# Kernel tuning notes

Hardware: AMD Instinct MI355X
Metric: run time of the kernel (lower is better)

## Reference

```python
import jax, jax.numpy as jnp
import numpy as np

B, C, H, W = 64, 256, 64, 64
E = 4                      # num_experts
CELL = 8
OUT = CELL * CELL + 1      # 65
EPS_BN = 1e-5
EPS_LB = 1e-6


def setup_inputs() -> dict:
    key = jax.random.key(0)
    ks = jax.random.split(key, 6)
    x = jax.random.normal(ks[0], (B, C, H, W), dtype=jnp.float32)
    w_experts = jax.random.normal(ks[1], (E, C, OUT), dtype=jnp.float32) * 0.05
    b_experts = jax.random.normal(ks[2], (E, OUT), dtype=jnp.float32) * 0.05
    w_gate = jax.random.normal(ks[3], (C, E), dtype=jnp.float32) * 0.05
    b_gate = jax.random.normal(ks[4], (E,), dtype=jnp.float32) * 0.05
    gamma = jnp.ones((OUT,), dtype=jnp.float32)
    beta = jnp.zeros((OUT,), dtype=jnp.float32)
    return {"x": x, "w_experts": w_experts, "b_experts": b_experts,
            "w_gate": w_gate, "b_gate": b_gate, "gamma": gamma, "beta": beta}


def pixel_shuffle(t, r):
    n, ch, h, w = t.shape
    nc = ch // (r * r)
    t = t.reshape(n, nc, r, r, h, w)
    t = t.transpose(0, 1, 4, 2, 5, 3)
    return t.reshape(n, nc, h * r, w * r)


def reference(x, w_experts, b_experts, w_gate, b_gate, gamma, beta):
    x = jax.nn.relu(x)
    xh = x.transpose(0, 2, 3, 1)                       # [B,H,W,C]

    # gating: global-avg-pool -> linear -> softmax -> hard top-1
    pooled = xh.mean(axis=(1, 2))                      # [B,C]
    gate = jax.nn.softmax(pooled @ w_gate + b_gate, axis=-1)
    idx = jnp.argmax(gate, axis=-1)                    # [B]

    # load-balancing KL(usage || uniform)
    usage = jnp.mean(jax.nn.one_hot(idx, E, dtype=xh.dtype), axis=0) + EPS_LB
    usage = usage / usage.sum()
    lb_loss = jnp.sum(usage * (jnp.log(usage) - jnp.log(jnp.full_like(usage, 1.0 / E))))

    # fused gather->grouped-GEMM (per-sample expert weight selection)
    w_sel = w_experts[idx]                             # [B,C,OUT]
    b_sel = b_experts[idx]                             # [B,OUT]
    y = jnp.einsum('bhwc,bco->bhwo', xh, w_sel) + b_sel[:, None, None, :]
    y = y.transpose(0, 3, 1, 2)                        # [B,OUT,H,W]

    # BatchNorm2d (training mode: batch statistics, biased variance)
    mean = y.mean(axis=(0, 2, 3), keepdims=True)
    var = y.var(axis=(0, 2, 3), keepdims=True)
    logits = (y - mean) / jnp.sqrt(var + EPS_BN)
    logits = logits * gamma[None, :, None, None] + beta[None, :, None, None]

    prob = jax.nn.softmax(logits, axis=1)[:, :-1]      # drop dustbin channel
    prob = pixel_shuffle(prob, CELL)                   # [B,1,H*8,W*8]
    prob = prob[:, 0]                                  # squeeze dim=1
    return logits, prob, lb_loss
```

## Files before the change

kernel.cpp:

```cpp
#include <hip/hip_runtime.h>
#include <stdint.h>
#include <math.h>

#define B_    64
#define C_    256
#define HW_   4096
#define E_    4
#define OUT_  65
#define NPAD_ 80

#define LOGITS_SZ (B_*OUT_*HW_)
#define PROB_SZ   (B_*512*512)

#define POOLED_OFF 0u
#define IDX_OFF    65536u
#define BNSUM_OFF  65792u
#define BNSS_OFF   66112u
#define SCSH_OFF   66432u
#define WT_OFF     67072u
#define YB_OFF     230912u
#define CLEAR_BYTES 66432u

typedef float  f4 __attribute__((ext_vector_type(4)));
typedef short  s8 __attribute__((ext_vector_type(8)));

__device__ __forceinline__ uint32_t f2bf(float f){
  uint32_t u = __float_as_uint(f);
  return (u + 0x7FFFu + ((u >> 16) & 1u)) >> 16;
}
__device__ __forceinline__ uint32_t pk(float lo, float hi){
  return f2bf(lo) | (f2bf(hi) << 16);
}
__device__ __forceinline__ float bf2f(uint32_t u){
  return __uint_as_float((u & 0xFFFFu) << 16);
}

__global__ __launch_bounds__(256) void k_prep(const float* __restrict__ x,
                                              uint16_t* __restrict__ xb,
                                              float* __restrict__ pooled){
  __shared__ float pool_lds[64];
  int bid = blockIdx.x;
  int b = bid >> 7, ct = (bid >> 5) & 3, pt = bid & 31;
  int t = threadIdx.x;
  int cg = t & 7, pgg = t >> 3;
  int c0 = ct*64 + cg*8;
  int p0 = pt*128 + pgg*4;
  if (t < 64) pool_lds[t] = 0.f;
  __syncthreads();

  float v[8][4]; float s[8];
  const float* xp = x + ((size_t)(b*C_ + c0))*HW_ + p0;
#pragma unroll
  for (int r = 0; r < 8; ++r){
    float4 f = *(const float4*)(xp + (size_t)r*HW_);
    v[r][0]=fmaxf(f.x,0.f); v[r][1]=fmaxf(f.y,0.f);
    v[r][2]=fmaxf(f.z,0.f); v[r][3]=fmaxf(f.w,0.f);
    s[r] = v[r][0]+v[r][1]+v[r][2]+v[r][3];
  }
  uint16_t* op = xb + ((size_t)(b*HW_ + p0))*C_ + c0;
#pragma unroll
  for (int p = 0; p < 4; ++p){
    uint4 w;
    w.x = pk(v[0][p], v[1][p]); w.y = pk(v[2][p], v[3][p]);
    w.z = pk(v[4][p], v[5][p]); w.w = pk(v[6][p], v[7][p]);
    *(uint4*)(op + (size_t)p*C_) = w;
  }
#pragma unroll
  for (int r = 0; r < 8; ++r){
    float vv = s[r];
    vv += __shfl_xor(vv, 8);
    vv += __shfl_xor(vv, 16);
    vv += __shfl_xor(vv, 32);
    if ((t & 56) == 0)
      atomicAdd(&pool_lds[cg*8 + r], vv);
  }
  __syncthreads();
  if (t < 64) atomicAdd(pooled + b*C_ + ct*64 + t, pool_lds[t]);
}

__global__ void k_wt(const float* __restrict__ w_experts, uint16_t* __restrict__ Wt){
  int bid = blockIdx.x;
  int e = bid / OUT_, o = bid % OUT_;
  int t = threadIdx.x, c = t*4;
  const float* src = w_experts + (size_t)e*C_*OUT_ + o;
  float a0 = src[(size_t)c*OUT_],     a1 = src[(size_t)(c+1)*OUT_];
  float a2 = src[(size_t)(c+2)*OUT_], a3 = src[(size_t)(c+3)*OUT_];
  uint2 w; w.x = pk(a0,a1); w.y = pk(a2,a3);
  *(uint2*)(Wt + ((size_t)(e*NPAD_ + o))*C_ + c) = w;
}

__global__ void k_gate(const float* __restrict__ pooled_sum,
                       const float* __restrict__ w_gate,
                       const float* __restrict__ b_gate,
                       int* __restrict__ idx_ws, float* __restrict__ out_lb){
  __shared__ float gl[64][4];
  __shared__ int ish[64];
  int t = threadIdx.x;
  int b = t >> 2, e = t & 3;
  float dot = 0.f;
  const float* pr = pooled_sum + b*C_;
  for (int c = 0; c < C_; c += 4){
    float4 p4 = *(const float4*)(pr + c);
    dot += p4.x*w_gate[c*4+e] + p4.y*w_gate[(c+1)*4+e]
         + p4.z*w_gate[(c+2)*4+e] + p4.w*w_gate[(c+3)*4+e];
  }
  gl[b][e] = dot * (1.f/4096.f) + b_gate[e];
  __syncthreads();
  if (t < 64){
    float best = gl[t][0]; int bi = 0;
    for (int ee = 1; ee < 4; ++ee){ float vv = gl[t][ee]; if (vv > best){best = vv; bi = ee;} }
    idx_ws[t] = bi; ish[t] = bi;
  }
  __syncthreads();
  if (t == 0){
    int cnt[4] = {0,0,0,0};
    for (int bb = 0; bb < 64; ++bb) cnt[ish[bb]]++;
    double u[4], S = 0.0;
    for (int ee = 0; ee < 4; ++ee){ u[ee] = cnt[ee]/64.0 + 1e-6; S += u[ee]; }
    double lb = 0.0;
    for (int ee = 0; ee < 4; ++ee){ double uu = u[ee]/S; lb += uu*(log(uu) - log(0.25)); }
    *out_lb = (float)lb;
  }
}

__global__ __launch_bounds__(256) void k_gemm(const uint16_t* __restrict__ xb,
                                              const uint16_t* __restrict__ Wt,
                                              const int* __restrict__ idx_ws,
                                              const float* __restrict__ b_experts,
                                              uint16_t* __restrict__ yb,
                                              float* __restrict__ bnsum,
                                              float* __restrict__ bnss){
  __shared__ float2 bnp[NPAD_*4];
  int bid = blockIdx.x;
  int b = bid >> 4, pt = bid & 15;
  int t = threadIdx.x;
  int w = t >> 6, lane = t & 63;
  int l15 = lane & 15, quad = lane >> 4;
  int e = idx_ws[b];
  int p0 = pt*256 + w*64;
  const uint16_t* ap = xb + ((size_t)(b*HW_ + p0 + l15))*C_ + quad*8;
  const uint16_t* bp = Wt + (size_t)e*NPAD_*C_ + (size_t)l15*C_ + quad*8;

  f4 acc[4][5];
#pragma unroll
  for (int mt=0; mt<4; ++mt)
#pragma unroll
    for (int nt=0; nt<5; ++nt){ f4 z = {0.f,0.f,0.f,0.f}; acc[mt][nt] = z; }

#pragma unroll
  for (int ks = 0; ks < 8; ++ks){
    int ko = ks*32;
    s8 av[4], bv[5];
#pragma unroll
    for (int mt=0; mt<4; ++mt) av[mt] = *(const s8*)(ap + (size_t)mt*16*C_ + ko);
#pragma unroll
    for (int nt=0; nt<5; ++nt) bv[nt] = *(const s8*)(bp + (size_t)nt*16*C_ + ko);
#pragma unroll
    for (int mt=0; mt<4; ++mt)
#pragma unroll
      for (int nt=0; nt<5; ++nt)
        acc[mt][nt] = __builtin_amdgcn_mfma_f32_16x16x32_bf16(av[mt], bv[nt], acc[mt][nt], 0, 0, 0);
  }

#pragma unroll
  for (int nt=0; nt<5; ++nt){
    int o = nt*16 + l15;
    float bias = (o < OUT_) ? b_experts[e*OUT_ + o] : 0.f;
    float s1 = 0.f, s2 = 0.f;
#pragma unroll
    for (int mt=0; mt<4; ++mt){
#pragma unroll
      for (int r=0; r<4; ++r){
        float vv = acc[mt][nt][r] + bias;
        acc[mt][nt][r] = vv;
        s1 += vv; s2 += vv*vv;
      }
      if (o < OUT_){
        size_t base = ((size_t)(b*OUT_ + o))*HW_ + p0 + mt*16 + quad*4;
        uint2 st;
        st.x = pk(acc[mt][nt][0], acc[mt][nt][1]);
        st.y = pk(acc[mt][nt][2], acc[mt][nt][3]);
        *(uint2*)(yb + base) = st;
      }
    }
    s1 += __shfl_xor(s1, 16); s1 += __shfl_xor(s1, 32);
    s2 += __shfl_xor(s2, 16); s2 += __shfl_xor(s2, 32);
    if (quad == 0) bnp[(nt*16 + l15)*4 + w] = make_float2(s1, s2);
  }
  __syncthreads();
  if (t < OUT_){
    float2 a0 = bnp[t*4+0], a1 = bnp[t*4+1], a2 = bnp[t*4+2], a3 = bnp[t*4+3];
    atomicAdd(bnsum + t, a0.x+a1.x+a2.x+a3.x);
    atomicAdd(bnss  + t, a0.y+a1.y+a2.y+a3.y);
  }
}

__global__ void k_stats(const float* __restrict__ bnsum, const float* __restrict__ bnss,
                        const float* __restrict__ gamma, const float* __restrict__ beta,
                        float2* __restrict__ scsh){
  int t = threadIdx.x;
  if (t < OUT_){
    const float invN = 1.f/(float)(B_*HW_);
    float mean = bnsum[t]*invN;
    float var  = bnss[t]*invN - mean*mean;
    float sc   = gamma[t] / sqrtf(var + 1e-5f);
    scsh[t] = make_float2(sc, beta[t] - mean*sc);
  }
}

__global__ __launch_bounds__(256) void k_final(const uint16_t* __restrict__ yb,
                                               const float2* __restrict__ scsh,
                                               float* __restrict__ out_logits,
                                               float* __restrict__ out_prob){
  __shared__ float lt[OUT_*132];
  __shared__ float2 ss[OUT_];
  int bid = blockIdx.x;
  int b = bid >> 5, pt = bid & 31;
  int p0 = pt*128;
  int t = threadIdx.x;
  if (t < OUT_) ss[t] = scsh[t];
  __syncthreads();

  int prr = t & 15, og = t >> 4;
#pragma unroll
  for (int oi = 0; oi < 5; ++oi){
    int o = og + oi*16;
    if (o < OUT_){
      size_t base = ((size_t)(b*OUT_ + o))*HW_ + p0 + prr*8;
      uint4 raw = *(const uint4*)(yb + base);
      float f[8];
      f[0]=bf2f(raw.x); f[1]=bf2f(raw.x>>16);
      f[2]=bf2f(raw.y); f[3]=bf2f(raw.y>>16);
      f[4]=bf2f(raw.z); f[5]=bf2f(raw.z>>16);
      f[6]=bf2f(raw.w); f[7]=bf2f(raw.w>>16);
      float2 sv = ss[o];
#pragma unroll
      for (int k=0;k<8;++k) f[k] = f[k]*sv.x + sv.y;
      float4 w0 = make_float4(f[0],f[1],f[2],f[3]);
      float4 w1 = make_float4(f[4],f[5],f[6],f[7]);
      *(float4*)(out_logits + base)     = w0;
      *(float4*)(out_logits + base + 4) = w1;
      float* lp = lt + o*132 + prr*8;
      *(float4*)(lp)     = w0;
      *(float4*)(lp + 4) = w1;
    }
  }
  __syncthreads();

  if (t < 128){
    float m = -1e30f;
    for (int o = 0; o < OUT_; ++o) m = fmaxf(m, lt[o*132 + t]);
    float ssum = 0.f;
    for (int o = 0; o < OUT_; ++o) ssum += __expf(lt[o*132 + t] - m);
    float inv = 1.f/ssum;
    int P = p0 + t;
    int h = P >> 6, wd = P & 63;
    float* pb = out_prob + ((size_t)b << 18) + (size_t)(h*8)*512 + wd*8;
#pragma unroll
    for (int r1 = 0; r1 < 8; ++r1){
      float4 q0, q1;
      q0.x = __expf(lt[(r1*8+0)*132+t]-m)*inv;
      q0.y = __expf(lt[(r1*8+1)*132+t]-m)*inv;
      q0.z = __expf(lt[(r1*8+2)*132+t]-m)*inv;
      q0.w = __expf(lt[(r1*8+3)*132+t]-m)*inv;
      q1.x = __expf(lt[(r1*8+4)*132+t]-m)*inv;
      q1.y = __expf(lt[(r1*8+5)*132+t]-m)*inv;
      q1.z = __expf(lt[(r1*8+6)*132+t]-m)*inv;
      q1.w = __expf(lt[(r1*8+7)*132+t]-m)*inv;
      *(float4*)(pb + r1*512)     = q0;
      *(float4*)(pb + r1*512 + 4) = q1;
    }
  }
}

extern "C" void kernel_launch(void* const* d_in, const int* in_sizes, int n_in,
                              void* d_out, int out_size, void* d_ws, size_t ws_size,
                              hipStream_t stream){
  const float* x         = (const float*)d_in[0];
  const float* w_experts = (const float*)d_in[1];
  const float* b_experts = (const float*)d_in[2];
  const float* w_gate    = (const float*)d_in[3];
  const float* b_gate    = (const float*)d_in[4];
  const float* gamma     = (const float*)d_in[5];
  const float* beta      = (const float*)d_in[6];

  float* out = (float*)d_out;
  char*  ws  = (char*)d_ws;
  float*     pooled = (float*)(ws + POOLED_OFF);
  int*       idxw   = (int*)(ws + IDX_OFF);
  float*     bnsum  = (float*)(ws + BNSUM_OFF);
  float*     bnss   = (float*)(ws + BNSS_OFF);
  float2*    scsh   = (float2*)(ws + SCSH_OFF);
  uint16_t*  Wt     = (uint16_t*)(ws + WT_OFF);
  uint16_t*  ybm    = (uint16_t*)(ws + YB_OFF);
  uint16_t*  xbm    = (uint16_t*)d_out;

  float* logits = out;
  float* prob   = out + LOGITS_SZ;
  float* lb     = out + LOGITS_SZ + PROB_SZ;

  hipMemsetAsync(ws, 0, CLEAR_BYTES, stream);
  k_prep <<<8192, 256, 0, stream>>>(x, xbm, pooled);
  k_wt   <<<E_*OUT_, 64, 0, stream>>>(w_experts, Wt);
  k_gate <<<1, 256, 0, stream>>>(pooled, w_gate, b_gate, idxw, lb);
  k_gemm <<<1024, 256, 0, stream>>>(xbm, Wt, idxw, b_experts, ybm, bnsum, bnss);
  k_stats<<<1, 128, 0, stream>>>(bnsum, bnss, gamma, beta, scsh);
  k_final<<<2048, 256, 0, stream>>>(ybm, scsh, logits, prob);
}
```

Before: 514.8 us.

## Pre-swizzle GEMM operands into MFMA fragment layout and merge small kernels

Writes the bf16 activations and expert weights in a fragment-major layout, so each wavefront's MFMA operand loads become contiguous 1 KB blocks instead of strided row reads. It also merges the weight-transpose and gating kernels into one launch and folds the BN stats kernel into k_final, removing two launches. The cost is more scattered stores in k_prep and the BN scale/shift being recomputed in every k_final block.

```diff
diff --git a/kernel.cpp b/kernel.cpp
--- a/kernel.cpp
+++ b/kernel.cpp
@@ -16,7 +16,6 @@
 #define IDX_OFF    65536u
 #define BNSUM_OFF  65792u
 #define BNSS_OFF   66112u
-#define SCSH_OFF   66432u
 #define WT_OFF     67072u
 #define YB_OFF     230912u
 #define CLEAR_BYTES 66432u
@@ -34,6 +33,7 @@
 __device__ __forceinline__ float bf2f(uint32_t u){
   return __uint_as_float((u & 0xFFFFu) << 16);
 }
+
 
 __global__ __launch_bounds__(256) void k_prep(const float* __restrict__ x,
                                               uint16_t* __restrict__ xb,
@@ -57,13 +57,17 @@
     v[r][2]=fmaxf(f.z,0.f); v[r][3]=fmaxf(f.w,0.f);
     s[r] = v[r][0]+v[r][1]+v[r][2]+v[r][3];
   }
-  uint16_t* op = xb + ((size_t)(b*HW_ + p0))*C_ + c0;
-#pragma unroll
-  for (int p = 0; p < 4; ++p){
+  int ksg  = ct*2 + (cg >> 2);
+  int quad = cg & 3;
+#pragma unroll
+  for (int pp = 0; pp < 4; ++pp){
+    int p = p0 + pp;
+    uint16_t* dst = xb + ((((size_t)(b*256 + (p>>4))*8 + ksg)*64)
+                          + (size_t)((p&15)*4 + quad))*8;
     uint4 w;
-    w.x = pk(v[0][p], v[1][p]); w.y = pk(v[2][p], v[3][p]);
-    w.z = pk(v[4][p], v[5][p]); w.w = pk(v[6][p], v[7][p]);
-    *(uint4*)(op + (size_t)p*C_) = w;
+    w.x = pk(v[0][pp], v[1][pp]); w.y = pk(v[2][pp], v[3][pp]);
+    w.z = pk(v[4][pp], v[5][pp]); w.w = pk(v[6][pp], v[7][pp]);
+    *(uint4*)dst = w;
   }
 #pragma unroll
   for (int r = 0; r < 8; ++r){
@@ -78,24 +82,39 @@
   if (t < 64) atomicAdd(pooled + b*C_ + ct*64 + t, pool_lds[t]);
 }
 
-__global__ void k_wt(const float* __restrict__ w_experts, uint16_t* __restrict__ Wt){
+__global__ void k_wtgate(const float* __restrict__ w_experts,
+                         const float* __restrict__ w_gate,
+                         const float* __restrict__ b_gate,
+                         const float* __restrict__ pooled_sum,
+                         uint16_t* __restrict__ Wt,
+                         int* __restrict__ idx_ws,
+                         float* __restrict__ out_lb){
   int bid = blockIdx.x;
-  int e = bid / OUT_, o = bid % OUT_;
-  int t = threadIdx.x, c = t*4;
-  const float* src = w_experts + (size_t)e*C_*OUT_ + o;
-  float a0 = src[(size_t)c*OUT_],     a1 = src[(size_t)(c+1)*OUT_];
-  float a2 = src[(size_t)(c+2)*OUT_], a3 = src[(size_t)(c+3)*OUT_];
-  uint2 w; w.x = pk(a0,a1); w.y = pk(a2,a3);
-  *(uint2*)(Wt + ((size_t)(e*NPAD_ + o))*C_ + c) = w;
-}
-
-__global__ void k_gate(const float* __restrict__ pooled_sum,
-                       const float* __restrict__ w_gate,
-                       const float* __restrict__ b_gate,
-                       int* __restrict__ idx_ws, float* __restrict__ out_lb){
+  int t = threadIdx.x;
+  if (bid < 320){
+    if (t >= 32) return;
+    int e = bid / NPAD_, o = bid % NPAD_;
+    int ks = t >> 2, quad = t & 3;
+    int c = t*8;
+    float a[8];
+    if (o < OUT_){
+      const float* src = w_experts + (size_t)e*C_*OUT_ + o;
+#pragma unroll
+      for (int j = 0; j < 8; ++j) a[j] = src[(size_t)(c+j)*OUT_];
+    } else {
+#pragma unroll
+      for (int j = 0; j < 8; ++j) a[j] = 0.f;
+    }
+    uint4 w;
+    w.x = pk(a[0],a[1]); w.y = pk(a[2],a[3]);
+    w.z = pk(a[4],a[5]); w.w = pk(a[6],a[7]);
+    uint16_t* dst = Wt + ((((size_t)(e*5 + (o>>4))*8 + ks)*64)
+                          + (size_t)((o&15)*4 + quad))*8;
+    *(uint4*)dst = w;
+    return;
+  }
   __shared__ float gl[64][4];
   __shared__ int ish[64];
-  int t = threadIdx.x;
   int b = t >> 2, e = t & 3;
   float dot = 0.f;
   const float* pr = pooled_sum + b*C_;
@@ -136,10 +155,11 @@
   int t = threadIdx.x;
   int w = t >> 6, lane = t & 63;
   int l15 = lane & 15, quad = lane >> 4;
+  int lid = l15*4 + quad;
   int e = idx_ws[b];
   int p0 = pt*256 + w*64;
-  const uint16_t* ap = xb + ((size_t)(b*HW_ + p0 + l15))*C_ + quad*8;
-  const uint16_t* bp = Wt + (size_t)e*NPAD_*C_ + (size_t)l15*C_ + quad*8;
+  const uint16_t* ap = xb + ((size_t)(b*256 + pt*16 + w*4))*4096 + (size_t)lid*8;
+  const uint16_t* bp = Wt + (size_t)e*5*4096 + (size_t)lid*8;
 
   f4 acc[4][5];
 #pragma unroll
@@ -149,12 +169,11 @@
 
 #pragma unroll
   for (int ks = 0; ks < 8; ++ks){
-    int ko = ks*32;
     s8 av[4], bv[5];
 #pragma unroll
-    for (int mt=0; mt<4; ++mt) av[mt] = *(const s8*)(ap + (size_t)mt*16*C_ + ko);
-#pragma unroll
-    for (int nt=0; nt<5; ++nt) bv[nt] = *(const s8*)(bp + (size_t)nt*16*C_ + ko);
+    for (int mt=0; mt<4; ++mt) av[mt] = *(const s8*)(ap + (size_t)mt*4096 + ks*512);
+#pragma unroll
+    for (int nt=0; nt<5; ++nt) bv[nt] = *(const s8*)(bp + (size_t)nt*4096 + ks*512);
 #pragma unroll
     for (int mt=0; mt<4; ++mt)
 #pragma unroll
@@ -195,21 +214,11 @@
   }
 }
 
-__global__ void k_stats(const float* __restrict__ bnsum, const float* __restrict__ bnss,
-                        const float* __restrict__ gamma, const float* __restrict__ beta,
-                        float2* __restrict__ scsh){
-  int t = threadIdx.x;
-  if (t < OUT_){
-    const float invN = 1.f/(float)(B_*HW_);
-    float mean = bnsum[t]*invN;
-    float var  = bnss[t]*invN - mean*mean;
-    float sc   = gamma[t] / sqrtf(var + 1e-5f);
-    scsh[t] = make_float2(sc, beta[t] - mean*sc);
-  }
-}
-
 __global__ __launch_bounds__(256) void k_final(const uint16_t* __restrict__ yb,
-                                               const float2* __restrict__ scsh,
+                                               const float* __restrict__ bnsum,
+                                               const float* __restrict__ bnss,
+                                               const float* __restrict__ gamma,
+                                               const float* __restrict__ beta,
                                                float* __restrict__ out_logits,
                                                float* __restrict__ out_prob){
   __shared__ float lt[OUT_*132];
@@ -218,7 +227,13 @@
   int b = bid >> 5, pt = bid & 31;
   int p0 = pt*128;
   int t = threadIdx.x;
-  if (t < OUT_) ss[t] = scsh[t];
+  if (t < OUT_){
+    const float invN = 1.f/(float)(B_*HW_);
+    float mean = bnsum[t]*invN;
+    float var  = bnss[t]*invN - mean*mean;
+    float sc   = gamma[t] / sqrtf(var + 1e-5f);
+    ss[t] = make_float2(sc, beta[t] - mean*sc);
+  }
   __syncthreads();
 
   int prr = t & 15, og = t >> 4;
@@ -290,7 +305,6 @@
   int*       idxw   = (int*)(ws + IDX_OFF);
   float*     bnsum  = (float*)(ws + BNSUM_OFF);
   float*     bnss   = (float*)(ws + BNSS_OFF);
-  float2*    scsh   = (float2*)(ws + SCSH_OFF);
   uint16_t*  Wt     = (uint16_t*)(ws + WT_OFF);
   uint16_t*  ybm    = (uint16_t*)(ws + YB_OFF);
   uint16_t*  xbm    = (uint16_t*)d_out;
@@ -300,10 +314,8 @@
   float* lb     = out + LOGITS_SZ + PROB_SZ;
 
   hipMemsetAsync(ws, 0, CLEAR_BYTES, stream);
-  k_prep <<<8192, 256, 0, stream>>>(x, xbm, pooled);
-  k_wt   <<<E_*OUT_, 64, 0, stream>>>(w_experts, Wt);
-  k_gate <<<1, 256, 0, stream>>>(pooled, w_gate, b_gate, idxw, lb);
-  k_gemm <<<1024, 256, 0, stream>>>(xbm, Wt, idxw, b_experts, ybm, bnsum, bnss);
-  k_stats<<<1, 128, 0, stream>>>(bnsum, bnss, gamma, beta, scsh);
-  k_final<<<2048, 256, 0, stream>>>(ybm, scsh, logits, prob);
-}
+  k_prep  <<<8192, 256, 0, stream>>>(x, xbm, pooled);
+  k_wtgate<<<321, 256, 0, stream>>>(w_experts, w_gate, b_gate, pooled, Wt, idxw, lb);
+  k_gemm  <<<1024, 256, 0, stream>>>(xbm, Wt, idxw, b_experts, ybm, bnsum, bnss);
+  k_final <<<2048, 256, 0, stream>>>(ybm, bnsum, bnss, gamma, beta, logits, prob);
+}
```

Measured after the change: 499.0 us. -3.1%, faster.
